# Kernel tuning notes

Hardware: AMD Instinct MI355X
Metric: run time of the kernel (lower is better)

## Reference

```python
import jax, jax.numpy as jnp
import numpy as np

EPSILON = 1e-06
MAXIMUM_AREA_RATIO = 0.3
GRID_HEIGHT = 160.0
CUBE = (25.0, 25.0, 32.0)
FEAT_SCALE = 1.0
GRID_SCALE = 1.0
CRANGE = (-1.0, 0.95)


def setup_inputs() -> dict:
    key = jax.random.key(0)
    k1, k2, k3, k4, k5 = jax.random.split(key, 5)
    B, C, H, W = 2, 256, 96, 320
    L, Wg = 128, 128
    n_layers = int(GRID_HEIGHT // CUBE[2])  # 5
    return {
        "feature": jax.random.normal(k1, (B, C, H, W), dtype=jnp.float32),
        "calib": jax.random.normal(k2, (B, 3, 4), dtype=jnp.float32),
        "grid": jax.random.normal(k3, (L, Wg, 3), dtype=jnp.float32),
        "Wc": jax.random.normal(k4, (C, C * n_layers), dtype=jnp.float32) * 0.02,
        "bc": jax.random.normal(k5, (C,), dtype=jnp.float32) * 0.02,
    }


def _cube_corners(cube):
    l, w, h = cube
    x = np.array([-l / 2, l / 2, l / 2, -l / 2, -l / 2, l / 2, l / 2, -l / 2])
    y = np.array([-w / 2, -w / 2, w / 2, w / 2, -w / 2, -w / 2, w / 2, w / 2])
    z = np.array([0, 0, 0, 0, h, h, h, h])
    return jnp.asarray(np.stack([x, y, z], axis=-1), dtype=jnp.float32)  # (8,3)


def _grid_sample_zeros(img, grd):
    # img: [B,C,H,W]; grd: [B,Hg,Wg,2] normalized coords in [-1,1]
    # bilinear, zero padding, align_corners=False (torch default)
    B, C, H, W = img.shape
    x = ((grd[..., 0] + 1.0) * W - 1.0) * 0.5
    y = ((grd[..., 1] + 1.0) * H - 1.0) * 0.5
    x0f = jnp.floor(x)
    y0f = jnp.floor(y)
    x0 = x0f.astype(jnp.int32)
    y0 = y0f.astype(jnp.int32)
    img_flat = img.reshape(B, C, H * W)

    def gather(xi, yi):
        valid = (xi >= 0) & (xi < W) & (yi >= 0) & (yi < H)
        xc = jnp.clip(xi, 0, W - 1)
        yc = jnp.clip(yi, 0, H - 1)
        idx = (yc * W + xc).reshape(B, 1, -1)
        v = jnp.take_along_axis(img_flat, idx, axis=2)
        v = v.reshape((B, C) + grd.shape[1:-1])
        return v * valid[:, None].astype(img.dtype)

    wx1 = x - x0f
    wx0 = 1.0 - wx1
    wy1 = y - y0f
    wy0 = 1.0 - wy1
    out = (gather(x0, y0) * (wx0 * wy0)[:, None]
           + gather(x0 + 1, y0) * (wx1 * wy0)[:, None]
           + gather(x0, y0 + 1) * (wx0 * wy1)[:, None]
           + gather(x0 + 1, y0 + 1) * (wx1 * wy1)[:, None])
    return out


def reference(feature, calib, grid, Wc, bc):
    B, C, H, W = feature.shape
    L, Wg, _ = grid.shape
    dtype = feature.dtype

    # z-layer offsets: (n_layers, 3) with offset only in z
    z_off = jnp.arange(0.0, GRID_HEIGHT, CUBE[2], dtype=dtype)  # (5,)
    n_layers = z_off.shape[0]
    z_corners = jnp.stack([jnp.zeros_like(z_off), jnp.zeros_like(z_off), z_off], axis=-1)
    offset = _cube_corners(CUBE)  # (8,3)

    # corners3d: (n_layers, L, Wg, 8, 3)
    corners = grid[None] + z_corners[:, None, None, :]  # (n,L,Wg,3)
    corners3d = (corners[:, :, :, None, :] + offset[None, None, None]) / GRID_SCALE

    # project with calib (B,3,4): homogeneous matmul then perspective divide
    hom = jnp.concatenate([corners3d, jnp.ones_like(corners3d[..., :1])], axis=-1)  # (n,L,Wg,8,4)
    pts = jnp.einsum('bij,nlwkj->bnlwki', calib, hom)  # (B,n,L,Wg,8,3)
    img_xy = pts[..., :2] / jnp.maximum(pts[..., 2:3], EPSILON)

    img_size = jnp.array([W, H], dtype=dtype) / FEAT_SCALE
    norm = jnp.clip(2.0 * img_xy / img_size - 1.0, CRANGE[0], CRANGE[1])  # (B,n,L,Wg,8,2)

    box_corners = jnp.concatenate([
        jnp.min(norm[..., 0], axis=-1, keepdims=True),
        jnp.min(norm[..., 1], axis=-1, keepdims=True),
        jnp.max(norm[..., 0], axis=-1, keepdims=True),
        jnp.max(norm[..., 1], axis=-1, keepdims=True),
    ], axis=-1)  # (B,n,L,Wg,4)
    box_corners = box_corners.reshape(B, n_layers, L * Wg, 4)

    area = ((box_corners[..., 2:] - box_corners[..., :2]).prod(axis=-1) * (H * W) + EPSILON)
    area = area[:, None]  # (B,1,n,LWg)
    visible = ((area > EPSILON) & (area < H * W * MAXIMUM_AREA_RATIO)).astype(dtype)

    integral = jnp.cumsum(jnp.cumsum(feature, axis=-1), axis=-2)

    lt = _grid_sample_zeros(integral, box_corners[..., [0, 1]])
    rb = _grid_sample_zeros(integral, box_corners[..., [2, 3]])
    rt = _grid_sample_zeros(integral, box_corners[..., [2, 1]])
    lb = _grid_sample_zeros(integral, box_corners[..., [0, 3]])

    vox = (lt + rb - rt - lb) / area * visible  # (B,C,n,LWg)
    # permute(0,3,1,2) -> (B, LWg, C, n); flatten to (B*LWg, C*n)
    vox = jnp.transpose(vox, (0, 3, 1, 2)).reshape(B * L * Wg, C * n_layers)

    ortho = vox @ Wc.T + bc  # (B*LWg, C)
    ortho = ortho.reshape(B, L, Wg, C)
    ortho = jax.nn.relu(jnp.transpose(ortho, (0, 3, 1, 2)))  # (B,C,L,Wg)
    return ortho
```

## Files before the change

kernel.cpp:

```cpp
#include <hip/hip_runtime.h>
#include <hip/hip_bf16.h>
#include <stdint.h>

#define BB 2
#define CC 256
#define HH 96
#define WW 320
#define NPIX 16384
#define NLAY 5
#define KDIM 1280
#define NDIM 32768
#define NKT (KDIM / 32)
#define NGRP 256

typedef float f32x4 __attribute__((ext_vector_type(4)));
typedef float f32x2 __attribute__((ext_vector_type(2)));
typedef __bf16 bf16x8 __attribute__((ext_vector_type(8)));
typedef __bf16 bf16x4 __attribute__((ext_vector_type(4)));

__global__ __launch_bounds__(1024) void k1f(const float* __restrict__ feat,
                                            float* __restrict__ integ,
                                            const float* __restrict__ gridp,
                                            const float* __restrict__ calib,
                                            const float* __restrict__ Wc,
                                            float4* __restrict__ coords,
                                            float* __restrict__ scales,
                                            __bf16* __restrict__ Wbf,
                                            uint8_t* __restrict__ mask8) {
  const int bid = blockIdx.x;
  if (bid < 480) {
    const int vbid = bid * 4 + (threadIdx.x >> 8);
    const int vt = threadIdx.x & 255;
    if (vbid >= 640) {
      int o = (vbid - 640) * 256 + vt;
      int co = o / KDIM;
      int kk = o % KDIM;
      int n = kk >> 8;
      int c = kk & 255;
      Wbf[o] = (__bf16)Wc[co * KDIM + c * NLAY + n];
      return;
    }
    int box = vbid * 256 + vt;
    int pix = box & (NPIX - 1);
    int bn = box >> 14;
    int n = bn % NLAY;
    int b = bn / NLAY;
    const float* cb = calib + b * 12;
    float c00 = cb[0], c01 = cb[1], c02 = cb[2], c03 = cb[3];
    float c10 = cb[4], c11 = cb[5], c12 = cb[6], c13 = cb[7];
    float c20 = cb[8], c21 = cb[9], c22 = cb[10], c23 = cb[11];
    float gx = gridp[pix * 3 + 0], gy = gridp[pix * 3 + 1], gz = gridp[pix * 3 + 2];
    float zoff = 32.0f * (float)n;
    const float ox[8] = {-12.5f, 12.5f, 12.5f, -12.5f, -12.5f, 12.5f, 12.5f, -12.5f};
    const float oy[8] = {-12.5f, -12.5f, 12.5f, 12.5f, -12.5f, -12.5f, 12.5f, 12.5f};
    float xmn = 1e30f, ymn = 1e30f, xmx = -1e30f, ymx = -1e30f;
#pragma unroll
    for (int k = 0; k < 8; ++k) {
      float X = gx + ox[k];
      float Y = gy + oy[k];
      float Z = gz + zoff + ((k >= 4) ? 32.0f : 0.0f);
      float px = c00 * X + c01 * Y + c02 * Z + c03;
      float py = c10 * X + c11 * Y + c12 * Z + c13;
      float pz = c20 * X + c21 * Y + c22 * Z + c23;
      float d = fmaxf(pz, 1e-6f);
      float nx = fminf(fmaxf(2.0f * (px / d) / 320.0f - 1.0f, -1.0f), 0.95f);
      float ny = fminf(fmaxf(2.0f * (py / d) / 96.0f - 1.0f, -1.0f), 0.95f);
      xmn = fminf(xmn, nx); xmx = fmaxf(xmx, nx);
      ymn = fminf(ymn, ny); ymx = fmaxf(ymx, ny);
    }
    float dx = xmx - xmn, dy = ymx - ymn;
    float area = (dx * dy) * 30720.0f + 1e-6f;
    bool vis = (area > 1e-6f) && (area < 9216.0f);
    {
      __shared__ uint32_t kf[16];
      unsigned long long bal = __ballot(vis);
      if ((threadIdx.x & 63) == 0) kf[threadIdx.x >> 6] = (bal != 0ull) ? 1u : 0u;
      __syncthreads();
      if (vt == 0) {
        int vb = threadIdx.x >> 8;
        int vbid2 = bid * 4 + vb;
        int bn2 = vbid2 >> 6;
        int n2 = bn2 % NLAY, b2 = bn2 / NLAY;
        int g0 = b2 * 128 + (vbid2 & 63) * 2;
        mask8[g0 * 5 + n2]       = (uint8_t)(kf[vb * 4 + 0] | kf[vb * 4 + 1]);
        mask8[(g0 + 1) * 5 + n2] = (uint8_t)(kf[vb * 4 + 2] | kf[vb * 4 + 3]);
      }
    }
    float X0 = ((xmn + 1.0f) * 320.0f - 1.0f) * 0.5f;
    float Y0 = ((ymn + 1.0f) * 96.0f - 1.0f) * 0.5f;
    float X1 = ((xmx + 1.0f) * 320.0f - 1.0f) * 0.5f;
    float Y1 = ((ymx + 1.0f) * 96.0f - 1.0f) * 0.5f;
    coords[box] = make_float4(X0, Y0, X1, Y1);
    scales[box] = vis ? 1.0f / area : 0.0f;
    return;
  }
  __shared__ float tile[WW * 33];
  const int t = threadIdx.x;
  const int wave = t >> 6;
  const int lane = t & 63;
  const int kb = bid - 480;
  const int cg = kb & 7;
  const int h = (kb >> 3) % HH;
  const int b = kb / (8 * HH);
  const int c0 = cg * 32;

  {
    const float* fb = feat + (size_t)((b * CC + c0) * HH + h) * WW;
    const size_t crstride = (size_t)HH * WW;
#pragma unroll
    for (int r = 0; r < 3; ++r) {
      int idx = r * 1024 + t;
      if (idx < 2560) {
        int cr = idx / 80;
        int wq = idx - cr * 80;
        f32x4 v = *(const f32x4*)(fb + cr * crstride + wq * 4);
        *(f32x4*)(&tile[cr * WW + wq * 4]) = v;
      }
    }
  }
  __syncthreads();
  const int ca = wave * 2, cbn = wave * 2 + 1;
  float va[5], vb[5];
#pragma unroll
  for (int j = 0; j < 5; ++j) va[j] = tile[ca * WW + lane * 5 + j];
#pragma unroll
  for (int j = 0; j < 5; ++j) vb[j] = tile[cbn * WW + lane * 5 + j];
#pragma unroll
  for (int j = 1; j < 5; ++j) { va[j] += va[j - 1]; vb[j] += vb[j - 1]; }
  float ta = va[4], tb = vb[4];
  float ia = ta, ib = tb;
#pragma unroll
  for (int d = 1; d < 64; d <<= 1) {
    float ua = __shfl_up(ia, d, 64);
    float ub = __shfl_up(ib, d, 64);
    if (lane >= d) { ia += ua; ib += ub; }
  }
  float pa = ia - ta, pb = ib - tb;
#pragma unroll
  for (int j = 0; j < 5; ++j) { va[j] += pa; vb[j] += pb; }
  __syncthreads();
#pragma unroll
  for (int j = 0; j < 5; ++j) {
    int w = lane * 5 + j;
    tile[w * 33 + ca]  = va[j];
    tile[w * 33 + cbn] = vb[j];
  }
  __syncthreads();
  float* dst = integ + (size_t)((b * HH + h) * WW) * CC + cg * 32;
#pragma unroll
  for (int r = 0; r < 3; ++r) {
    int idx = r * 1024 + t;
    if (idx < 2560) {
      int w = idx >> 3;
      int cq = (idx & 7) * 4;
      float4 o = make_float4(tile[w * 33 + cq + 0], tile[w * 33 + cq + 1],
                             tile[w * 33 + cq + 2], tile[w * 33 + cq + 3]);
      *(float4*)(dst + (size_t)w * CC + cq) = o;
    }
  }
}

__global__ __launch_bounds__(256) void k2_scan(float* __restrict__ integ) {
  const int blk = blockIdx.x;
  const int w = blk % WW;
  const int b = blk / WW;
  const int g = threadIdx.x >> 6;
  const int l = threadIdx.x & 63;
  float* base = integ + ((size_t)(b * HH + g * 24) * WW + w) * CC + l * 4;
  const size_t stride = (size_t)WW * CC;
  f32x4 v[24];
#pragma unroll
  for (int i = 0; i < 24; ++i) v[i] = *(const f32x4*)(base + (size_t)i * stride);
#pragma unroll
  for (int i = 1; i < 24; ++i) v[i] += v[i - 1];
  __shared__ f32x4 part[4][64];
  part[g][l] = v[23];
  __syncthreads();
  f32x4 off = {0.f, 0.f, 0.f, 0.f};
#pragma unroll
  for (int gg = 0; gg < 3; ++gg)
    if (gg < g) off += part[gg][l];
#pragma unroll
  for (int i = 0; i < 24; ++i) *(f32x4*)(base + (size_t)i * stride) = v[i] + off;
}

__global__ __launch_bounds__(256) void k4_vox(const float* __restrict__ integ,
                                              const float4* __restrict__ coords,
                                              const float* __restrict__ scales,
                                              __bf16* __restrict__ voxA,
                                              const uint8_t* __restrict__ mask8) {
  const int wave = threadIdx.x >> 6;
  const int lane = threadIdx.x & 63;
  const int box0 = (blockIdx.x * 4 + wave) * 4;
  {
    const int pix0 = box0 & (NPIX - 1);
    const int bn0 = box0 >> 14;
    const int n0 = bn0 % NLAY, b0 = bn0 / NLAY;
    if (mask8[((b0 * NPIX + pix0) >> 7) * 5 + n0] == 0) return;
  }
#pragma unroll
  for (int u = 0; u < 4; ++u) {
    const int box = box0 + u;
    const int pix = box & (NPIX - 1);
    const int bn = box >> 14;
    const int n = bn % NLAY;
    const int b = bn / NLAY;
    const size_t row = (size_t)(b * NPIX + pix);
    bf16x4* dst = (bf16x4*)(voxA + row * KDIM + n * CC + lane * 4);
    const float scale = scales[box];
    if (scale == 0.f) {
      *dst = bf16x4{(__bf16)0.f, (__bf16)0.f, (__bf16)0.f, (__bf16)0.f};
      continue;
    }
    const float4 q = coords[box];

    float xw[4]; int xi[4];
    float yw[4]; int yi[4];
    {
      float f0 = floorf(q.x); int i0 = (int)f0; float w1 = q.x - f0;
      xw[0] = (i0 >= 0 && i0 < WW) ? (1.f - w1) : 0.f;
      xw[1] = (i0 + 1 < WW) ? w1 : 0.f;
      xi[0] = min(max(i0, 0), WW - 1); xi[1] = min(max(i0 + 1, 0), WW - 1);
      float f1 = floorf(q.z); int i1 = (int)f1; float v1 = q.z - f1;
      xw[2] = (i1 >= 0 && i1 < WW) ? -(1.f - v1) : 0.f;
      xw[3] = (i1 + 1 < WW) ? -v1 : 0.f;
      xi[2] = min(max(i1, 0), WW - 1); xi[3] = min(max(i1 + 1, 0), WW - 1);
    }
    {
      float f0 = floorf(q.y); int j0 = (int)f0; float w1 = q.y - f0;
      yw[0] = (j0 >= 0 && j0 < HH) ? (1.f - w1) : 0.f;
      yw[1] = (j0 + 1 < HH) ? w1 : 0.f;
      yi[0] = min(max(j0, 0), HH - 1); yi[1] = min(max(j0 + 1, 0), HH - 1);
      float f1 = floorf(q.w); int j1 = (int)f1; float v1 = q.w - f1;
      yw[2] = (j1 >= 0 && j1 < HH) ? -(1.f - v1) : 0.f;
      yw[3] = (j1 + 1 < HH) ? -v1 : 0.f;
      yi[2] = min(max(j1, 0), HH - 1); yi[3] = min(max(j1 + 1, 0), HH - 1);
    }
    const float* base = integ + (size_t)(b * HH) * WW * CC + lane * 4;
    f32x4 val = {0.f, 0.f, 0.f, 0.f};
#pragma unroll
    for (int jj = 0; jj < 4; ++jj) {
      if (yw[jj] == 0.f) continue;
      const float* rp = base + (size_t)yi[jj] * WW * CC;
      f32x4 rs = {0.f, 0.f, 0.f, 0.f};
#pragma unroll
      for (int ii = 0; ii < 4; ++ii) {
        if (xw[ii] != 0.f) {
          f32x4 v = *(const f32x4*)(rp + (size_t)xi[ii] * CC);
          rs += xw[ii] * v;
        }
      }
      val += yw[jj] * rs;
    }
    val *= scale;
    *dst = bf16x4{(__bf16)val.x, (__bf16)val.y, (__bf16)val.z, (__bf16)val.w};
  }
}

__device__ __forceinline__ void glds16(const void* g, void* l) {
  __builtin_amdgcn_global_load_lds(
      (const __attribute__((address_space(1))) void*)g,
      (__attribute__((address_space(3))) void*)(uint32_t)(uintptr_t)l,
      16, 0, 0);
}

__global__ __launch_bounds__(256) void k6_gemm(const __bf16* __restrict__ A,
                                               const __bf16* __restrict__ Bm,
                                               const float* __restrict__ bias,
                                               float* __restrict__ out,
                                               const uint8_t* __restrict__ mask8) {
  __shared__ __align__(16) __bf16 As[4][128 * 32];
  __shared__ __align__(16) __bf16 Bs[4][128 * 32];
  __shared__ uint8_t ktsS[NKT];
  __shared__ int LsS;
  const int tileM = blockIdx.y * 128;
  const int tileN = blockIdx.x * 128;
  const int tid = threadIdx.x;
  const int lane = tid & 63;
  const int wave = tid >> 6;
  const int wm = (wave >> 1) * 64;
  const int wn = (wave & 1) * 64;

  if (tid == 0) {
    const uint8_t* mg = mask8 + blockIdx.x * 5;
    int L = 0;
#pragma unroll
    for (int n = 0; n < NLAY; ++n)
      if (mg[n]) {
#pragma unroll
        for (int kk = 0; kk < 8; ++kk) ktsS[L++] = (uint8_t)(n * 8 + kk);
      }
    LsS = L;
  }

  f32x4 acc[4][4];
#pragma unroll
  for (int i = 0; i < 4; ++i)
#pragma unroll
    for (int j = 0; j < 4; ++j)
      acc[i][j] = f32x4{0.f, 0.f, 0.f, 0.f};

  const int r16 = lane & 15;
  const int q4 = lane >> 4;
  const int srow = (lane >> 2);
  const int sch = lane & 3;

  auto stage = [&](int buf, int kt) {
    const int k0 = kt * 32;
#pragma unroll
    for (int rr = 0; rr < 2; ++rr) {
      const int base_row = wave * 16 + rr * 64;
      const int row = base_row + srow;
      const int gch = sch ^ ((row >> 1) & 3);
      glds16(A  + (size_t)(tileM + row) * KDIM + k0 + gch * 8,
             (void*)(&As[buf][base_row * 32] + lane * 8));
      glds16(Bm + (size_t)(tileN + row) * KDIM + k0 + gch * 8,
             (void*)(&Bs[buf][base_row * 32] + lane * 8));
    }
  };

  __syncthreads();
  const int L = LsS;
#pragma unroll
  for (int s = 0; s < 3; ++s)
    if (s < L) stage(s, ktsS[s]);
  for (int i = 0; i < L; ++i) {
    const int cur = i & 3;
    const int rem = L - i;
    if (rem >= 3)      __builtin_amdgcn_s_waitcnt(0xF78);
    else if (rem == 2) __builtin_amdgcn_s_waitcnt(0xF74);
    else               __builtin_amdgcn_s_waitcnt(0xF70);
    __builtin_amdgcn_s_barrier();
    if (i + 3 < L) stage((i + 3) & 3, ktsS[i + 3]);
    bf16x8 af[4], bg[4];
#pragma unroll
    for (int ii = 0; ii < 4; ++ii) {
      int m = wm + ii * 16 + r16;
      af[ii] = *(const bf16x8*)(&As[cur][m * 32] + (q4 ^ ((m >> 1) & 3)) * 8);
    }
#pragma unroll
    for (int j = 0; j < 4; ++j) {
      int nr = wn + j * 16 + r16;
      bg[j] = *(const bf16x8*)(&Bs[cur][nr * 32] + (q4 ^ ((nr >> 1) & 3)) * 8);
    }
#pragma unroll
    for (int ii = 0; ii < 4; ++ii)
#pragma unroll
      for (int j = 0; j < 4; ++j)
        acc[ii][j] = __builtin_amdgcn_mfma_f32_16x16x32_bf16(af[ii], bg[j], acc[ii][j], 0, 0, 0);
  }

#pragma unroll
  for (int i = 0; i < 4; ++i) {
#pragma unroll
    for (int j = 0; j < 4; ++j) {
      int nn = tileN + wn + j * 16 + r16;
      int bI = nn >> 14;
      int pix = nn & (NPIX - 1);
#pragma unroll
      for (int r = 0; r < 4; ++r) {
        int co = tileM + wm + i * 16 + q4 * 4 + r;
        float v = acc[i][j][r] + bias[co];
        out[(size_t)(bI * CC + co) * NPIX + pix] = fmaxf(v, 0.f);
      }
    }
  }
}

extern "C" void kernel_launch(void* const* d_in, const int* in_sizes, int n_in,
                              void* d_out, int out_size, void* d_ws, size_t ws_size,
                              hipStream_t stream) {
  const float* feat  = (const float*)d_in[0];
  const float* calib = (const float*)d_in[1];
  const float* grid  = (const float*)d_in[2];
  const float* Wc    = (const float*)d_in[3];
  const float* bc    = (const float*)d_in[4];
  float* out = (float*)d_out;

  char* ws = (char*)d_ws;
  const size_t SZ_INTEG = (size_t)BB * HH * WW * CC * 4;
  const size_t SZ_VOX   = (size_t)NDIM * KDIM * 2;
  const size_t SZ_WBF   = (size_t)CC * KDIM * 2;
  const size_t SZ_CRD   = (size_t)BB * NLAY * NPIX * 16;
  const size_t SZ_SCL   = (size_t)BB * NLAY * NPIX * 4;
  const size_t SZ_MSK   = (size_t)NGRP * NLAY;
  if (ws_size < SZ_INTEG + SZ_VOX + SZ_WBF + SZ_CRD + SZ_SCL + SZ_MSK) return;

  float*   integ  = (float*)ws;
  __bf16*  voxA   = (__bf16*)(ws + SZ_INTEG);
  __bf16*  Wbf    = (__bf16*)(ws + SZ_INTEG + SZ_VOX);
  float4*  coords = (float4*)(ws + SZ_INTEG + SZ_VOX + SZ_WBF);
  float*   scales = (float*)(ws + SZ_INTEG + SZ_VOX + SZ_WBF + SZ_CRD);
  uint8_t* mask8  = (uint8_t*)(ws + SZ_INTEG + SZ_VOX + SZ_WBF + SZ_CRD + SZ_SCL);

  k1f<<<dim3(BB * HH * 8 + 480), dim3(1024), 0, stream>>>(
      feat, integ, grid, calib, Wc, coords, scales, Wbf, mask8);
  k2_scan<<<dim3(BB * WW), dim3(256), 0, stream>>>(integ);
  k4_vox<<<dim3(BB * NLAY * NPIX / 16), dim3(256), 0, stream>>>(integ, coords, scales, voxA, mask8);
  k6_gemm<<<dim3(NDIM / 128, 2), dim3(256), 0, stream>>>(Wbf, voxA, bc, out, mask8);
}
```

Baseline: 160.3 us.

## Fuse box-filter voxel sampling into GEMM, building B tiles in LDS

Merges the voxel sampling kernel and the GEMM into one kernel. Each block computes the voxel features for 128 pixels of one active layer straight into a padded LDS tile, then runs MFMA against the weight tiles streamed with global_load_lds. This removes the bf16 voxel buffer round-trip through global memory and one launch. The cost is only 256 blocks of 512 threads with a large LDS footprint, and sampling is serialized with the GEMM inside each block, which may lower occupancy and latency hiding.

```diff
diff --git a/kernel.cpp b/kernel.cpp
--- a/kernel.cpp
+++ b/kernel.cpp
@@ -12,6 +12,7 @@
 #define NDIM 32768
 #define NKT (KDIM / 32)
 #define NGRP 256
+#define BSP 264
 
 typedef float f32x4 __attribute__((ext_vector_type(4)));
 typedef float f32x2 __attribute__((ext_vector_type(2)));
@@ -184,79 +185,6 @@
   for (int i = 0; i < 24; ++i) *(f32x4*)(base + (size_t)i * stride) = v[i] + off;
 }
 
-__global__ __launch_bounds__(256) void k4_vox(const float* __restrict__ integ,
-                                              const float4* __restrict__ coords,
-                                              const float* __restrict__ scales,
-                                              __bf16* __restrict__ voxA,
-                                              const uint8_t* __restrict__ mask8) {
-  const int wave = threadIdx.x >> 6;
-  const int lane = threadIdx.x & 63;
-  const int box0 = (blockIdx.x * 4 + wave) * 4;
-  {
-    const int pix0 = box0 & (NPIX - 1);
-    const int bn0 = box0 >> 14;
-    const int n0 = bn0 % NLAY, b0 = bn0 / NLAY;
-    if (mask8[((b0 * NPIX + pix0) >> 7) * 5 + n0] == 0) return;
-  }
-#pragma unroll
-  for (int u = 0; u < 4; ++u) {
-    const int box = box0 + u;
-    const int pix = box & (NPIX - 1);
-    const int bn = box >> 14;
-    const int n = bn % NLAY;
-    const int b = bn / NLAY;
-    const size_t row = (size_t)(b * NPIX + pix);
-    bf16x4* dst = (bf16x4*)(voxA + row * KDIM + n * CC + lane * 4);
-    const float scale = scales[box];
-    if (scale == 0.f) {
-      *dst = bf16x4{(__bf16)0.f, (__bf16)0.f, (__bf16)0.f, (__bf16)0.f};
-      continue;
-    }
-    const float4 q = coords[box];
-
-    float xw[4]; int xi[4];
-    float yw[4]; int yi[4];
-    {
-      float f0 = floorf(q.x); int i0 = (int)f0; float w1 = q.x - f0;
-      xw[0] = (i0 >= 0 && i0 < WW) ? (1.f - w1) : 0.f;
-      xw[1] = (i0 + 1 < WW) ? w1 : 0.f;
-      xi[0] = min(max(i0, 0), WW - 1); xi[1] = min(max(i0 + 1, 0), WW - 1);
-      float f1 = floorf(q.z); int i1 = (int)f1; float v1 = q.z - f1;
-      xw[2] = (i1 >= 0 && i1 < WW) ? -(1.f - v1) : 0.f;
-      xw[3] = (i1 + 1 < WW) ? -v1 : 0.f;
-      xi[2] = min(max(i1, 0), WW - 1); xi[3] = min(max(i1 + 1, 0), WW - 1);
-    }
-    {
-      float f0 = floorf(q.y); int j0 = (int)f0; float w1 = q.y - f0;
-      yw[0] = (j0 >= 0 && j0 < HH) ? (1.f - w1) : 0.f;
-      yw[1] = (j0 + 1 < HH) ? w1 : 0.f;
-      yi[0] = min(max(j0, 0), HH - 1); yi[1] = min(max(j0 + 1, 0), HH - 1);
-      float f1 = floorf(q.w); int j1 = (int)f1; float v1 = q.w - f1;
-      yw[2] = (j1 >= 0 && j1 < HH) ? -(1.f - v1) : 0.f;
-      yw[3] = (j1 + 1 < HH) ? -v1 : 0.f;
-      yi[2] = min(max(j1, 0), HH - 1); yi[3] = min(max(j1 + 1, 0), HH - 1);
-    }
-    const float* base = integ + (size_t)(b * HH) * WW * CC + lane * 4;
-    f32x4 val = {0.f, 0.f, 0.f, 0.f};
-#pragma unroll
-    for (int jj = 0; jj < 4; ++jj) {
-      if (yw[jj] == 0.f) continue;
-      const float* rp = base + (size_t)yi[jj] * WW * CC;
-      f32x4 rs = {0.f, 0.f, 0.f, 0.f};
-#pragma unroll
-      for (int ii = 0; ii < 4; ++ii) {
-        if (xw[ii] != 0.f) {
-          f32x4 v = *(const f32x4*)(rp + (size_t)xi[ii] * CC);
-          rs += xw[ii] * v;
-        }
-      }
-      val += yw[jj] * rs;
-    }
-    val *= scale;
-    *dst = bf16x4{(__bf16)val.x, (__bf16)val.y, (__bf16)val.z, (__bf16)val.w};
-  }
-}
-
 __device__ __forceinline__ void glds16(const void* g, void* l) {
   __builtin_amdgcn_global_load_lds(
       (const __attribute__((address_space(1))) void*)g,
@@ -264,34 +192,30 @@
       16, 0, 0);
 }
 
-__global__ __launch_bounds__(256) void k6_gemm(const __bf16* __restrict__ A,
-                                               const __bf16* __restrict__ Bm,
-                                               const float* __restrict__ bias,
-                                               float* __restrict__ out,
-                                               const uint8_t* __restrict__ mask8) {
-  __shared__ __align__(16) __bf16 As[4][128 * 32];
-  __shared__ __align__(16) __bf16 Bs[4][128 * 32];
-  __shared__ uint8_t ktsS[NKT];
-  __shared__ int LsS;
-  const int tileM = blockIdx.y * 128;
-  const int tileN = blockIdx.x * 128;
+__global__ __launch_bounds__(512) void k46(const __bf16* __restrict__ A,
+                                           const float* __restrict__ integ,
+                                           const float4* __restrict__ coords,
+                                           const float* __restrict__ scales,
+                                           const float* __restrict__ bias,
+                                           float* __restrict__ out,
+                                           const uint8_t* __restrict__ mask8) {
+  __shared__ __align__(16) __bf16 As[3][256 * 32];
+  __shared__ __align__(16) __bf16 Bs[128 * BSP];
+  const int g = blockIdx.x;
+  const int b = g >> 7;
+  const int pix0 = (g & 127) * 128;
   const int tid = threadIdx.x;
   const int lane = tid & 63;
   const int wave = tid >> 6;
   const int wm = (wave >> 1) * 64;
   const int wn = (wave & 1) * 64;
-
-  if (tid == 0) {
-    const uint8_t* mg = mask8 + blockIdx.x * 5;
-    int L = 0;
-#pragma unroll
-    for (int n = 0; n < NLAY; ++n)
-      if (mg[n]) {
-#pragma unroll
-        for (int kk = 0; kk < 8; ++kk) ktsS[L++] = (uint8_t)(n * 8 + kk);
-      }
-    LsS = L;
-  }
+  const int r16 = lane & 15;
+  const int q4 = lane >> 4;
+
+  int ln[NLAY], nact = 0;
+#pragma unroll
+  for (int n = 0; n < NLAY; ++n)
+    if (mask8[g * 5 + n]) ln[nact++] = n;
 
   f32x4 acc[4][4];
 #pragma unroll
@@ -300,68 +224,113 @@
     for (int j = 0; j < 4; ++j)
       acc[i][j] = f32x4{0.f, 0.f, 0.f, 0.f};
 
-  const int r16 = lane & 15;
-  const int q4 = lane >> 4;
-  const int srow = (lane >> 2);
-  const int sch = lane & 3;
-
   auto stage = [&](int buf, int kt) {
     const int k0 = kt * 32;
 #pragma unroll
     for (int rr = 0; rr < 2; ++rr) {
-      const int base_row = wave * 16 + rr * 64;
-      const int row = base_row + srow;
-      const int gch = sch ^ ((row >> 1) & 3);
-      glds16(A  + (size_t)(tileM + row) * KDIM + k0 + gch * 8,
+      const int base_row = rr * 128 + wave * 16;
+      const int row = base_row + (lane >> 2);
+      const int gch = (lane & 3) ^ ((row >> 1) & 3);
+      glds16(A + (size_t)row * KDIM + k0 + gch * 8,
              (void*)(&As[buf][base_row * 32] + lane * 8));
-      glds16(Bm + (size_t)(tileN + row) * KDIM + k0 + gch * 8,
-             (void*)(&Bs[buf][base_row * 32] + lane * 8));
     }
   };
 
-  __syncthreads();
-  const int L = LsS;
-#pragma unroll
-  for (int s = 0; s < 3; ++s)
-    if (s < L) stage(s, ktsS[s]);
-  for (int i = 0; i < L; ++i) {
-    const int cur = i & 3;
-    const int rem = L - i;
-    if (rem >= 3)      __builtin_amdgcn_s_waitcnt(0xF78);
-    else if (rem == 2) __builtin_amdgcn_s_waitcnt(0xF74);
-    else               __builtin_amdgcn_s_waitcnt(0xF70);
-    __builtin_amdgcn_s_barrier();
-    if (i + 3 < L) stage((i + 3) & 3, ktsS[i + 3]);
-    bf16x8 af[4], bg[4];
-#pragma unroll
-    for (int ii = 0; ii < 4; ++ii) {
-      int m = wm + ii * 16 + r16;
-      af[ii] = *(const bf16x8*)(&As[cur][m * 32] + (q4 ^ ((m >> 1) & 3)) * 8);
-    }
+  for (int la = 0; la < nact; ++la) {
+    const int n = ln[la];
+    const int bn = b * NLAY + n;
+    const float* gbase = integ + (size_t)(b * HH) * WW * CC + lane * 4;
+#pragma unroll 4
+    for (int u = 0; u < 16; ++u) {
+      const int row = wave * 16 + u;
+      const int box = (bn << 14) | (pix0 + row);
+      bf16x4* dst = (bf16x4*)(&Bs[row * BSP + lane * 4]);
+      const float scale = scales[box];
+      if (scale == 0.f) {
+        *dst = bf16x4{(__bf16)0.f, (__bf16)0.f, (__bf16)0.f, (__bf16)0.f};
+        continue;
+      }
+      const float4 q = coords[box];
+      float xw[4]; int xi[4];
+      float yw[4]; int yi[4];
+      {
+        float f0 = floorf(q.x); int i0 = (int)f0; float w1 = q.x - f0;
+        xw[0] = (i0 >= 0 && i0 < WW) ? (1.f - w1) : 0.f;
+        xw[1] = (i0 + 1 < WW) ? w1 : 0.f;
+        xi[0] = min(max(i0, 0), WW - 1); xi[1] = min(max(i0 + 1, 0), WW - 1);
+        float f1 = floorf(q.z); int i1 = (int)f1; float v1 = q.z - f1;
+        xw[2] = (i1 >= 0 && i1 < WW) ? -(1.f - v1) : 0.f;
+        xw[3] = (i1 + 1 < WW) ? -v1 : 0.f;
+        xi[2] = min(max(i1, 0), WW - 1); xi[3] = min(max(i1 + 1, 0), WW - 1);
+      }
+      {
+        float f0 = floorf(q.y); int j0 = (int)f0; float w1 = q.y - f0;
+        yw[0] = (j0 >= 0 && j0 < HH) ? (1.f - w1) : 0.f;
+        yw[1] = (j0 + 1 < HH) ? w1 : 0.f;
+        yi[0] = min(max(j0, 0), HH - 1); yi[1] = min(max(j0 + 1, 0), HH - 1);
+        float f1 = floorf(q.w); int j1 = (int)f1; float v1 = q.w - f1;
+        yw[2] = (j1 >= 0 && j1 < HH) ? -(1.f - v1) : 0.f;
+        yw[3] = (j1 + 1 < HH) ? -v1 : 0.f;
+        yi[2] = min(max(j1, 0), HH - 1); yi[3] = min(max(j1 + 1, 0), HH - 1);
+      }
+      f32x4 val = {0.f, 0.f, 0.f, 0.f};
+#pragma unroll
+      for (int jj = 0; jj < 4; ++jj) {
+        if (yw[jj] == 0.f) continue;
+        const float* rp = gbase + (size_t)yi[jj] * WW * CC;
+        f32x4 rs = {0.f, 0.f, 0.f, 0.f};
+#pragma unroll
+        for (int ii = 0; ii < 4; ++ii) {
+          if (xw[ii] != 0.f) {
+            f32x4 v = *(const f32x4*)(rp + (size_t)xi[ii] * CC);
+            rs += xw[ii] * v;
+          }
+        }
+        val += yw[jj] * rs;
+      }
+      val *= scale;
+      *dst = bf16x4{(__bf16)val.x, (__bf16)val.y, (__bf16)val.z, (__bf16)val.w};
+    }
+    __syncthreads();
+    const int base = n * 8;
+    stage(0, base);
+    stage(1, base + 1);
+    for (int kk = 0; kk < 8; ++kk) {
+      const int cur = kk % 3;
+      if (kk < 7) __builtin_amdgcn_s_waitcnt(0xF72);
+      else        __builtin_amdgcn_s_waitcnt(0xF70);
+      __builtin_amdgcn_s_barrier();
+      if (kk + 2 < 8) stage((kk + 2) % 3, base + kk + 2);
+      bf16x8 af[4], bg[4];
+#pragma unroll
+      for (int i = 0; i < 4; ++i) {
+        int m = wm + i * 16 + r16;
+        af[i] = *(const bf16x8*)(&As[cur][m * 32] + (q4 ^ ((m >> 1) & 3)) * 8);
+      }
+#pragma unroll
+      for (int j = 0; j < 4; ++j) {
+        int nr = wn + j * 16 + r16;
+        bg[j] = *(const bf16x8*)(&Bs[nr * BSP + kk * 32 + q4 * 8]);
+      }
+#pragma unroll
+      for (int i = 0; i < 4; ++i)
+#pragma unroll
+        for (int j = 0; j < 4; ++j)
+          acc[i][j] = __builtin_amdgcn_mfma_f32_16x16x32_bf16(af[i], bg[j], acc[i][j], 0, 0, 0);
+    }
+    __syncthreads();
+  }
+
+#pragma unroll
+  for (int i = 0; i < 4; ++i) {
 #pragma unroll
     for (int j = 0; j < 4; ++j) {
-      int nr = wn + j * 16 + r16;
-      bg[j] = *(const bf16x8*)(&Bs[cur][nr * 32] + (q4 ^ ((nr >> 1) & 3)) * 8);
-    }
-#pragma unroll
-    for (int ii = 0; ii < 4; ++ii)
-#pragma unroll
-      for (int j = 0; j < 4; ++j)
-        acc[ii][j] = __builtin_amdgcn_mfma_f32_16x16x32_bf16(af[ii], bg[j], acc[ii][j], 0, 0, 0);
-  }
-
-#pragma unroll
-  for (int i = 0; i < 4; ++i) {
-#pragma unroll
-    for (int j = 0; j < 4; ++j) {
-      int nn = tileN + wn + j * 16 + r16;
-      int bI = nn >> 14;
-      int pix = nn & (NPIX - 1);
+      int pix = pix0 + wn + j * 16 + r16;
 #pragma unroll
       for (int r = 0; r < 4; ++r) {
-        int co = tileM + wm + i * 16 + q4 * 4 + r;
+        int co = wm + i * 16 + q4 * 4 + r;
         float v = acc[i][j][r] + bias[co];
-        out[(size_t)(bI * CC + co) * NPIX + pix] = fmaxf(v, 0.f);
+        out[(size_t)(b * CC + co) * NPIX + pix] = fmaxf(v, 0.f);
       }
     }
   }
@@ -387,7 +356,6 @@
   if (ws_size < SZ_INTEG + SZ_VOX + SZ_WBF + SZ_CRD + SZ_SCL + SZ_MSK) return;
 
   float*   integ  = (float*)ws;
-  __bf16*  voxA   = (__bf16*)(ws + SZ_INTEG);
   __bf16*  Wbf    = (__bf16*)(ws + SZ_INTEG + SZ_VOX);
   float4*  coords = (float4*)(ws + SZ_INTEG + SZ_VOX + SZ_WBF);
   float*   scales = (float*)(ws + SZ_INTEG + SZ_VOX + SZ_WBF + SZ_CRD);
@@ -396,6 +364,5 @@
   k1f<<<dim3(BB * HH * 8 + 480), dim3(1024), 0, stream>>>(
       feat, integ, grid, calib, Wc, coords, scales, Wbf, mask8);
   k2_scan<<<dim3(BB * WW), dim3(256), 0, stream>>>(integ);
-  k4_vox<<<dim3(BB * NLAY * NPIX / 16), dim3(256), 0, stream>>>(integ, coords, scales, voxA, mask8);
-  k6_gemm<<<dim3(NDIM / 128, 2), dim3(256), 0, stream>>>(Wbf, voxA, bc, out, mask8);
-}
+  k46<<<dim3(NGRP), dim3(512), 0, stream>>>(Wbf, integ, coords, scales, bc, out, mask8);
+}
```

New measurement: 193.0 us. 1.2x slower.
